# Kernel optimization log

Measured on AMD Instinct MI355X. Metric: run time of the kernel, lower is better.

Reference implementation:

```python
import jax, jax.numpy as jnp
import numpy as np

NEG_BIG = -9e15

def setup_inputs() -> dict:
    key = jax.random.key(0)
    kx, ka, kW, k1, k2 = jax.random.split(key, 5)
    B, N, F, H, D = 8, 1024, 1024, 16, 64
    x = jax.random.normal(kx, (B, N, F), dtype=jnp.float32)
    adj = jax.random.randint(ka, (B, N, N), 0, 2, dtype=jnp.int32)
    # xavier_uniform with gain=1.414
    gain = 1.414
    limW = gain * np.sqrt(6.0 / (F + D))
    lima = gain * np.sqrt(6.0 / (D + 1))
    W = jax.random.uniform(kW, (H, F, D), minval=-limW, maxval=limW, dtype=jnp.float32)
    a1 = jax.random.uniform(k1, (H, D), minval=-lima, maxval=lima, dtype=jnp.float32)
    a2 = jax.random.uniform(k2, (H, D), minval=-lima, maxval=lima, dtype=jnp.float32)
    return {"x": x, "adj": adj, "W": W, "a1": a1, "a2": a2}

def reference(x, adj, W, a1, a2):
    alpha = 0.2
    # Wh: [B, H, N, D]
    Wh = jnp.einsum('bnf,hfd->bhnd', x, W)
    f1 = jnp.einsum('bhnd,hd->bhn', Wh, a1)  # [B,H,N]
    f2 = jnp.einsum('bhnd,hd->bhn', Wh, a2)  # [B,H,N]
    e = f1[:, :, :, None] + f2[:, :, None, :]          # [B,H,N,N]
    e = jnp.where(e > 0, e, alpha * e)                  # leaky relu
    mask = (adj > 0)[:, None, :, :]                     # [B,1,N,N]
    scores = jnp.where(mask, e, NEG_BIG)
    attn = jax.nn.softmax(scores, axis=-1)              # [B,H,N,N]
    # dropout omitted (inference / training=False)
    h_prime = jnp.einsum('bhnm,bhmd->bhnd', attn, Wh)   # [B,H,N,D]
    B, H, N, D = h_prime.shape
    # concat heads along feature dim (matches torch.cat over dim=2)
    y = jnp.transpose(h_prime, (0, 2, 1, 3)).reshape(B, N, H * D)
    return y
```

## Files before the change

kernel.cpp:

```cpp
#include <hip/hip_runtime.h>

typedef float    f32x4 __attribute__((ext_vector_type(4)));
typedef short    s16x8 __attribute__((ext_vector_type(8)));
typedef _Float16 f16x8 __attribute__((ext_vector_type(8)));
typedef _Float16 f16x4 __attribute__((ext_vector_type(4)));
typedef unsigned int   u32x4 __attribute__((ext_vector_type(4)));


__device__ __forceinline__ unsigned short bf16rne(float f){
  unsigned u = __float_as_uint(f);
  return (unsigned short)((u + 0x7FFFu + ((u >> 16) & 1u)) >> 16);
}

__global__ __launch_bounds__(256) void prep_kernel(const int* __restrict__ adj,
    const float* __restrict__ x, const float* __restrict__ W,
    unsigned* __restrict__ maskb, unsigned short* __restrict__ xb,
    unsigned short* __restrict__ Wt)
{
  const int bid = blockIdx.x, tid = threadIdx.x;
  if (bid < 1024) {
    const int lane = tid & 63;
    int gw = (bid * 256 + tid) >> 6;
    for (int s = gw; s < 131072; s += 4096) {
      int a = adj[(size_t)s * 64 + lane];
      unsigned long long m = __ballot(a > 0);
      if (lane == 0) {
        maskb[s * 2]     = (unsigned)m;
        maskb[s * 2 + 1] = (unsigned)(m >> 32);
      }
    }
  } else if (bid < 5120) {
    int idx = ((bid - 1024) * 256 + tid) * 8;
    f32x4 v0 = *reinterpret_cast<const f32x4*>(&x[idx]);
    f32x4 v1 = *reinterpret_cast<const f32x4*>(&x[idx + 4]);
    u32x4 o;
    o[0] = (unsigned)bf16rne(v0[0]) | ((unsigned)bf16rne(v0[1]) << 16);
    o[1] = (unsigned)bf16rne(v0[2]) | ((unsigned)bf16rne(v0[3]) << 16);
    o[2] = (unsigned)bf16rne(v1[0]) | ((unsigned)bf16rne(v1[1]) << 16);
    o[3] = (unsigned)bf16rne(v1[2]) | ((unsigned)bf16rne(v1[3]) << 16);
    *reinterpret_cast<u32x4*>(&xb[idx]) = o;
  } else {
    __shared__ float t[16][17];
    int rel = bid - 5120;
    int f0 = (rel & 63) * 16, d0 = ((rel >> 6) & 3) * 16, hh = rel >> 8;
    const int tx = tid & 15, ty = tid >> 4;
    t[ty][tx] = W[(size_t)hh * 65536 + (size_t)(f0 + ty) * 64 + (d0 + tx)];
    __syncthreads();
    float v = t[tx][ty];
    size_t o = (size_t)(hh * 64 + d0 + ty) * 1024 + (f0 + tx);
    Wt[o] = bf16rne(v);
  }
}

__global__ __launch_bounds__(256, 3) void gemm_kernel(const unsigned short* __restrict__ xb,
    const unsigned short* __restrict__ Btg,
    const float* __restrict__ a1, const float* __restrict__ a2,
    _Float16* __restrict__ WhT, float* __restrict__ f1, float* __restrict__ f2)
{
  __shared__ unsigned short Ah[128 * 40], Bh[128 * 40];
  const int tid  = threadIdx.x;
  const int lane = tid & 63, wave = tid >> 6;
  const int m0 = blockIdx.x * 128, n0 = blockIdx.y * 128;
  const int wm = (wave & 1) * 64, wn = (wave >> 1) * 64;
  const int rA = lane & 15, kg = lane >> 4;

  f32x4 acc[4][4] = {};

  for (int k0 = 0; k0 < 1024; k0 += 32) {
#pragma unroll
    for (int r = 0; r < 2; ++r) {
      int flat = r * 256 + tid;
      int row = flat >> 2;
      int o8  = (flat & 3) << 3;
      *reinterpret_cast<u32x4*>(&Ah[row * 40 + o8]) =
          *reinterpret_cast<const u32x4*>(&xb[(size_t)(m0 + row) * 1024 + k0 + o8]);
    }
#pragma unroll
    for (int r = 0; r < 2; ++r) {
      int flat = r * 256 + tid;
      int row = flat >> 2;
      int o8  = (flat & 3) << 3;
      *reinterpret_cast<u32x4*>(&Bh[row * 40 + o8]) =
          *reinterpret_cast<const u32x4*>(&Btg[(size_t)(n0 + row) * 1024 + k0 + o8]);
    }
    __syncthreads();

    s16x8 ah[4], bh[4];
#pragma unroll
    for (int i = 0; i < 4; ++i)
      ah[i] = *reinterpret_cast<const s16x8*>(&Ah[(wm + i * 16 + rA) * 40 + kg * 8]);
#pragma unroll
    for (int j = 0; j < 4; ++j)
      bh[j] = *reinterpret_cast<const s16x8*>(&Bh[(wn + j * 16 + rA) * 40 + kg * 8]);
#pragma unroll
    for (int i = 0; i < 4; ++i)
#pragma unroll
      for (int j = 0; j < 4; ++j)
        acc[i][j] = __builtin_amdgcn_mfma_f32_16x16x32_bf16(ah[i], bh[j], acc[i][j], 0, 0, 0);
    __syncthreads();
  }

#pragma unroll
  for (int i = 0; i < 4; ++i) {
    int gm0 = m0 + wm + i * 16 + kg * 4;
#pragma unroll
    for (int j = 0; j < 4; ++j) {
      int gn = n0 + wn + j * 16 + rA;
      int bb = gm0 >> 10, nn = gm0 & 1023;
      int hh = gn >> 6,  dd = gn & 63;
      f16x4 hv;
#pragma unroll
      for (int jj = 0; jj < 4; ++jj) hv[jj] = (_Float16)acc[i][j][jj];
      *reinterpret_cast<f16x4*>(&WhT[((size_t)((bb * 16 + hh) * 64 + dd) << 10) + nn]) = hv;
    }
  }

  const int hw = (n0 + wn) >> 6;
  float a1v[4], a2v[4];
#pragma unroll
  for (int j = 0; j < 4; ++j) {
    int d = j * 16 + rA;
    a1v[j] = a1[hw * 64 + d];
    a2v[j] = a2[hw * 64 + d];
  }
#pragma unroll
  for (int i = 0; i < 4; ++i) {
#pragma unroll
    for (int jj = 0; jj < 4; ++jj) {
      float s1 = 0.f, s2 = 0.f;
#pragma unroll
      for (int j = 0; j < 4; ++j) {
        float v = acc[i][j][jj];
        s1 += v * a1v[j];
        s2 += v * a2v[j];
      }
#pragma unroll
      for (int off = 1; off < 16; off <<= 1) {
        s1 += __shfl_xor(s1, off);
        s2 += __shfl_xor(s2, off);
      }
      if (rA == 0) {
        int gm = m0 + wm + i * 16 + kg * 4 + jj;
        int bb = gm >> 10, nn = gm & 1023;
        size_t o = (size_t)(bb * 16 + hw) * 1024 + nn;
        f1[o] = s1;
        f2[o] = s2;
      }
    }
  }
}

__global__ __launch_bounds__(256, 4) void pv_kernel(const _Float16* __restrict__ WhT,
    const float* __restrict__ f1, const float* __restrict__ f2,
    const unsigned* __restrict__ maskb, float* __restrict__ y)
{
  const int tid = threadIdx.x, lane = tid & 63, wave = tid >> 6;
  const int rb = blockIdx.x, h = blockIdx.y, b = blockIdx.z;
  const int bh = b * 16 + h;
  const int n0 = rb * 64;
  const _Float16* whtb = WhT + ((size_t)bh << 16);

  __shared__ _Float16 Bsh[64 * 72];
  __shared__ float Cs[1024], Ds[1024];
  __shared__ float smx[4];
  __shared__ unsigned long long lutm[16];

  const float K = 1.44269504f;

  float pmax;
  {
    f32x4 fv = *reinterpret_cast<const f32x4*>(&f2[(size_t)bh * 1024 + tid * 4]);
    f32x4 sv, cv, dv;
#pragma unroll
    for (int e = 0; e < 4; ++e) {
      sv[e] = fv[e] * K;
      cv[e] = __builtin_amdgcn_exp2f(sv[e]);
      dv[e] = __builtin_amdgcn_exp2f(0.2f * sv[e]);
    }
    *reinterpret_cast<f32x4*>(&Cs[tid * 4]) = cv;
    *reinterpret_cast<f32x4*>(&Ds[tid * 4]) = dv;
    pmax = fmaxf(fmaxf(sv[0], sv[1]), fmaxf(sv[2], sv[3]));
  }
#pragma unroll
  for (int off = 32; off; off >>= 1) pmax = fmaxf(pmax, __shfl_xor(pmax, off));
  if (lane == 0) smx[wave] = pmax;
  if (tid < 16) {
    unsigned lo = ((tid & 1) ? 0xFFFFu : 0u) | ((tid & 2) ? 0xFFFF0000u : 0u);
    unsigned hi = ((tid & 4) ? 0xFFFFu : 0u) | ((tid & 8) ? 0xFFFF0000u : 0u);
    lutm[tid] = ((unsigned long long)hi << 32) | lo;
  }
  __syncthreads();

  const float m2s = fmaxf(fmaxf(smx[0], smx[1]), fmaxf(smx[2], smx[3]));

  const int rA = lane & 15, kg = lane >> 4;
  const int wrow = wave * 16;
  f32x4 acc[4] = {};
  f32x4 dacc = {};
  const int rloc = wrow + rA;
  float At, Bt;
  {
    float f1p = f1[(size_t)bh * 1024 + n0 + rloc] * K;
    float sf = f1p + m2s;
    float Mp = fmaxf(sf, 0.2f * sf);
    At = __builtin_amdgcn_exp2f(f1p - Mp);
    Bt = __builtin_amdgcn_exp2f(0.2f * f1p - Mp);
  }
  const unsigned* mrow = maskb + ((size_t)(b << 10) + n0 + rloc) * 32;
  f16x8 ones;
#pragma unroll
  for (int e = 0; e < 8; ++e) ones[e] = (_Float16)1.0f;

  for (int m0 = 0; m0 < 1024; m0 += 64) {
    uint2 mw2 = *reinterpret_cast<const uint2*>(&mrow[m0 >> 5]);
#pragma unroll
    for (int r = 0; r < 2; ++r) {
      int flat = r * 256 + tid;
      int d = flat >> 3, o = (flat & 7) << 3;
      *reinterpret_cast<u32x4*>(&Bsh[d * 72 + o]) =
          *reinterpret_cast<const u32x4*>(&whtb[(size_t)d * 1024 + m0 + o]);
    }
    __syncthreads();
#pragma unroll
    for (int ks = 0; ks < 2; ++ks) {
      const int kc = m0 + ks * 32 + kg * 8;
      f32x4 ca = *reinterpret_cast<const f32x4*>(&Cs[kc]);
      f32x4 cb = *reinterpret_cast<const f32x4*>(&Cs[kc + 4]);
      f32x4 da = *reinterpret_cast<const f32x4*>(&Ds[kc]);
      f32x4 db = *reinterpret_cast<const f32x4*>(&Ds[kc + 4]);
      unsigned mw = (&mw2.x)[ks] >> (kg * 8);
      f16x8 pa;
#pragma unroll
      for (int jj = 0; jj < 8; ++jj) {
        float C = (jj < 4) ? ca[jj] : cb[jj - 4];
        float D = (jj < 4) ? da[jj] : db[jj - 4];
        pa[jj] = (_Float16)fmaxf(At * C, Bt * D);
      }
      u32x4 pw = __builtin_bit_cast(u32x4, pa);
      unsigned long long mq0 = lutm[mw & 15u];
      unsigned long long mq1 = lutm[(mw >> 4) & 15u];
      pw[0] &= (unsigned)mq0;  pw[1] &= (unsigned)(mq0 >> 32);
      pw[2] &= (unsigned)mq1;  pw[3] &= (unsigned)(mq1 >> 32);
      pa = __builtin_bit_cast(f16x8, pw);
      dacc = __builtin_amdgcn_mfma_f32_16x16x32_f16(pa, ones, dacc, 0, 0, 0);
#pragma unroll
      for (int j = 0; j < 4; ++j) {
        f16x8 bf = *reinterpret_cast<const f16x8*>(&Bsh[(j * 16 + rA) * 72 + ks * 32 + kg * 8]);
        acc[j] = __builtin_amdgcn_mfma_f32_16x16x32_f16(pa, bf, acc[j], 0, 0, 0);
      }
    }
    __syncthreads();
  }

  f32x4 rd;
#pragma unroll
  for (int jj = 0; jj < 4; ++jj) rd[jj] = dacc[jj] > 0.f ? 1.0f / dacc[jj] : 0.f;
#pragma unroll
  for (int j = 0; j < 4; ++j) {
#pragma unroll
    for (int jj = 0; jj < 4; ++jj) {
      int row = wrow + kg * 4 + jj;
      int n = n0 + row, d = j * 16 + rA;
      y[(((size_t)b * 1024 + n) << 10) + h * 64 + d] = acc[j][jj] * rd[jj];
    }
  }
}

extern "C" void kernel_launch(void* const* d_in, const int* in_sizes, int n_in,
                              void* d_out, int out_size, void* d_ws, size_t ws_size,
                              hipStream_t stream)
{
  const float* x  = (const float*)d_in[0];
  const int*   adj = (const int*)d_in[1];
  const float* W  = (const float*)d_in[2];
  const float* a1 = (const float*)d_in[3];
  const float* a2 = (const float*)d_in[4];
  float* y = (float*)d_out;

  char* ws = (char*)d_ws;
  unsigned short* Wt = (unsigned short*)(ws);
  unsigned*       maskb = (unsigned*)(ws + ((size_t)2 << 20));
  float* f1   = (float*)(ws + ((size_t)3 << 20));
  float* f2   = (float*)(ws + ((size_t)3 << 20) + ((size_t)512 << 10));
  _Float16* WhT = (_Float16*)(ws + ((size_t)4 << 20));
  unsigned short* xb = (unsigned short*)(ws + ((size_t)20 << 20));

  prep_kernel<<<9216, 256, 0, stream>>>(adj, x, W, maskb, xb, Wt);
  gemm_kernel<<<dim3(64, 8), 256, 0, stream>>>(xb, Wt, a1, a2, WhT, f1, f2);
  pv_kernel<<<dim3(16, 16, 8), 256, 0, stream>>>(WhT, f1, f2, maskb, y);
}
```

Before: 99.43 us.

## Load PV B-fragments directly from global into registers with double buffering

Drops the shared-memory staging of the WhT tile and its two barriers per iteration. Each lane now reads its MFMA B-operand fragments straight from global memory into registers, with a two-stage register double buffer so the next tile's loads overlap the current tile's MFMAs. This removes LDS traffic and synchronisation, but each wave now fetches the full B tile itself, so global/L2 reads rise fourfold and register pressure grows.

```diff
diff --git a/kernel.cpp b/kernel.cpp
--- a/kernel.cpp
+++ b/kernel.cpp
@@ -150,6 +150,62 @@
   }
 }
 
+#define PVLOAD(da, db, mdst, M0) \
+  { _Pragma("unroll") \
+    for (int j = 0; j < 4; ++j) { \
+      da[j] = *reinterpret_cast<const f16x8*>(&bbase[j * 16384 + (M0)]); \
+      db[j] = *reinterpret_cast<const f16x8*>(&bbase[j * 16384 + (M0) + 32]); \
+    } \
+    mdst = *reinterpret_cast<const uint2*>(&mrow[(M0) >> 5]); }
+
+#define PVCOMP(M0, Fa, Fb, MW) \
+  { { const int kc = (M0) + kg * 8; \
+      f32x4 ca = *reinterpret_cast<const f32x4*>(&Cs[kc]); \
+      f32x4 cb = *reinterpret_cast<const f32x4*>(&Cs[kc + 4]); \
+      f32x4 da = *reinterpret_cast<const f32x4*>(&Ds[kc]); \
+      f32x4 db = *reinterpret_cast<const f32x4*>(&Ds[kc + 4]); \
+      unsigned mw = MW.x >> (kg * 8); \
+      f16x8 pa; \
+      _Pragma("unroll") \
+      for (int jj = 0; jj < 8; ++jj) { \
+        float C = (jj < 4) ? ca[jj] : cb[jj - 4]; \
+        float D = (jj < 4) ? da[jj] : db[jj - 4]; \
+        pa[jj] = (_Float16)fmaxf(At * C, Bt * D); \
+      } \
+      u32x4 pw = __builtin_bit_cast(u32x4, pa); \
+      unsigned long long mq0 = lutm[mw & 15u]; \
+      unsigned long long mq1 = lutm[(mw >> 4) & 15u]; \
+      pw[0] &= (unsigned)mq0;  pw[1] &= (unsigned)(mq0 >> 32); \
+      pw[2] &= (unsigned)mq1;  pw[3] &= (unsigned)(mq1 >> 32); \
+      pa = __builtin_bit_cast(f16x8, pw); \
+      dacc = __builtin_amdgcn_mfma_f32_16x16x32_f16(pa, ones, dacc, 0, 0, 0); \
+      _Pragma("unroll") \
+      for (int j = 0; j < 4; ++j) \
+        acc[j] = __builtin_amdgcn_mfma_f32_16x16x32_f16(pa, Fa[j], acc[j], 0, 0, 0); } \
+    { const int kc = (M0) + 32 + kg * 8; \
+      f32x4 ca = *reinterpret_cast<const f32x4*>(&Cs[kc]); \
+      f32x4 cb = *reinterpret_cast<const f32x4*>(&Cs[kc + 4]); \
+      f32x4 da = *reinterpret_cast<const f32x4*>(&Ds[kc]); \
+      f32x4 db = *reinterpret_cast<const f32x4*>(&Ds[kc + 4]); \
+      unsigned mw = MW.y >> (kg * 8); \
+      f16x8 pa; \
+      _Pragma("unroll") \
+      for (int jj = 0; jj < 8; ++jj) { \
+        float C = (jj < 4) ? ca[jj] : cb[jj - 4]; \
+        float D = (jj < 4) ? da[jj] : db[jj - 4]; \
+        pa[jj] = (_Float16)fmaxf(At * C, Bt * D); \
+      } \
+      u32x4 pw = __builtin_bit_cast(u32x4, pa); \
+      unsigned long long mq0 = lutm[mw & 15u]; \
+      unsigned long long mq1 = lutm[(mw >> 4) & 15u]; \
+      pw[0] &= (unsigned)mq0;  pw[1] &= (unsigned)(mq0 >> 32); \
+      pw[2] &= (unsigned)mq1;  pw[3] &= (unsigned)(mq1 >> 32); \
+      pa = __builtin_bit_cast(f16x8, pw); \
+      dacc = __builtin_amdgcn_mfma_f32_16x16x32_f16(pa, ones, dacc, 0, 0, 0); \
+      _Pragma("unroll") \
+      for (int j = 0; j < 4; ++j) \
+        acc[j] = __builtin_amdgcn_mfma_f32_16x16x32_f16(pa, Fb[j], acc[j], 0, 0, 0); } }
+
 __global__ __launch_bounds__(256, 4) void pv_kernel(const _Float16* __restrict__ WhT,
     const float* __restrict__ f1, const float* __restrict__ f2,
     const unsigned* __restrict__ maskb, float* __restrict__ y)
@@ -160,7 +216,6 @@
   const int n0 = rb * 64;
   const _Float16* whtb = WhT + ((size_t)bh << 16);
 
-  __shared__ _Float16 Bsh[64 * 72];
   __shared__ float Cs[1024], Ds[1024];
   __shared__ float smx[4];
   __shared__ unsigned long long lutm[16];
@@ -207,49 +262,20 @@
     Bt = __builtin_amdgcn_exp2f(0.2f * f1p - Mp);
   }
   const unsigned* mrow = maskb + ((size_t)(b << 10) + n0 + rloc) * 32;
+  const _Float16* bbase = whtb + (size_t)rA * 1024 + kg * 8;
   f16x8 ones;
 #pragma unroll
   for (int e = 0; e < 8; ++e) ones[e] = (_Float16)1.0f;
 
-  for (int m0 = 0; m0 < 1024; m0 += 64) {
-    uint2 mw2 = *reinterpret_cast<const uint2*>(&mrow[m0 >> 5]);
-#pragma unroll
-    for (int r = 0; r < 2; ++r) {
-      int flat = r * 256 + tid;
-      int d = flat >> 3, o = (flat & 7) << 3;
-      *reinterpret_cast<u32x4*>(&Bsh[d * 72 + o]) =
-          *reinterpret_cast<const u32x4*>(&whtb[(size_t)d * 1024 + m0 + o]);
-    }
-    __syncthreads();
-#pragma unroll
-    for (int ks = 0; ks < 2; ++ks) {
-      const int kc = m0 + ks * 32 + kg * 8;
-      f32x4 ca = *reinterpret_cast<const f32x4*>(&Cs[kc]);
-      f32x4 cb = *reinterpret_cast<const f32x4*>(&Cs[kc + 4]);
-      f32x4 da = *reinterpret_cast<const f32x4*>(&Ds[kc]);
-      f32x4 db = *reinterpret_cast<const f32x4*>(&Ds[kc + 4]);
-      unsigned mw = (&mw2.x)[ks] >> (kg * 8);
-      f16x8 pa;
-#pragma unroll
-      for (int jj = 0; jj < 8; ++jj) {
-        float C = (jj < 4) ? ca[jj] : cb[jj - 4];
-        float D = (jj < 4) ? da[jj] : db[jj - 4];
-        pa[jj] = (_Float16)fmaxf(At * C, Bt * D);
-      }
-      u32x4 pw = __builtin_bit_cast(u32x4, pa);
-      unsigned long long mq0 = lutm[mw & 15u];
-      unsigned long long mq1 = lutm[(mw >> 4) & 15u];
-      pw[0] &= (unsigned)mq0;  pw[1] &= (unsigned)(mq0 >> 32);
-      pw[2] &= (unsigned)mq1;  pw[3] &= (unsigned)(mq1 >> 32);
-      pa = __builtin_bit_cast(f16x8, pw);
-      dacc = __builtin_amdgcn_mfma_f32_16x16x32_f16(pa, ones, dacc, 0, 0, 0);
-#pragma unroll
-      for (int j = 0; j < 4; ++j) {
-        f16x8 bf = *reinterpret_cast<const f16x8*>(&Bsh[(j * 16 + rA) * 72 + ks * 32 + kg * 8]);
-        acc[j] = __builtin_amdgcn_mfma_f32_16x16x32_f16(pa, bf, acc[j], 0, 0, 0);
-      }
-    }
-    __syncthreads();
+  f16x8 Xa[4], Xb[4], Ya[4], Yb[4];
+  uint2 mX, mY;
+
+  PVLOAD(Xa, Xb, mX, 0);
+  for (int m0 = 0; m0 < 1024; m0 += 128) {
+    PVLOAD(Ya, Yb, mY, m0 + 64);
+    PVCOMP(m0, Xa, Xb, mX);
+    if (m0 + 128 < 1024) { PVLOAD(Xa, Xb, mX, m0 + 128); }
+    PVCOMP(m0 + 64, Ya, Yb, mY);
   }
 
   f32x4 rd;
```

After: 184.5 us. 85.6% more time.
